# Kernel optimization log

Hardware: AMD Instinct MI355X
Metric: run time of the kernel (lower is better)

## Reference

```python
import jax, jax.numpy as jnp
import numpy as np

HEADS = 16
HEAD_DIM = 64
DIM = 1024
INNER = HEADS * HEAD_DIM  # 1024


def rotate_half(t):
    # split last dim into two halves, return cat(-x2, x1)
    x1, x2 = jnp.split(t, 2, axis=-1)
    return jnp.concatenate((-x2, x1), axis=-1)


def rope_table(n, head_dim, dtype):
    inv_freq = 1.0 / (10000.0 ** (jnp.arange(0, head_dim, 2, dtype=jnp.float32) / head_dim))
    freqs = jnp.arange(n, dtype=jnp.float32)[:, None] * inv_freq[None, :]  # [n, hd/2]
    return jnp.concatenate((freqs, freqs), axis=-1).astype(dtype)  # [n, hd]


def setup_inputs() -> dict:
    key = jax.random.key(0)
    k1, k2, k3, k4 = jax.random.split(key, 4)
    x = jax.random.normal(k1, (1, 4096, DIM), dtype=jnp.float32)
    s = 0.02
    W_qkv = jax.random.normal(k2, (DIM, 3 * INNER), dtype=jnp.float32) * s
    W_o1 = jax.random.normal(k3, (INNER, DIM), dtype=jnp.float32) * s
    W_o2 = jax.random.normal(k4, (DIM, DIM), dtype=jnp.float32) * s
    gamma = jnp.ones((DIM,), dtype=jnp.float32)
    return {"x": x, "W_qkv": W_qkv, "W_o1": W_o1, "W_o2": W_o2, "gamma": gamma}


def reference(x, W_qkv, W_o1, W_o2, gamma):
    b, n, _ = x.shape
    scale = HEAD_DIM ** -0.5
    qkv = x @ W_qkv  # [b, n, 3*inner]
    q, k, v = jnp.split(qkv, 3, axis=-1)
    # [b, n, inner] -> [b, h, n, hd]
    to_heads = lambda t: t.reshape(b, n, HEADS, HEAD_DIM).transpose(0, 2, 1, 3)
    q, k, v = to_heads(q), to_heads(k), to_heads(v)

    pos = rope_table(n, HEAD_DIM, x.dtype)  # [n, hd]
    cos, sin = jnp.cos(pos), jnp.sin(pos)
    apply_rope = lambda t: t * cos + rotate_half(t) * sin
    q, k = apply_rope(q), apply_rope(k)

    dots = jnp.einsum('bhid,bhjd->bhij', q, k) * scale  # [b, h, n, n]
    causal = jnp.triu(jnp.ones((n, n), dtype=bool), 1)
    neg = -jnp.finfo(dots.dtype).max
    dots = jnp.where(causal, neg, dots)
    attn = jax.nn.softmax(dots, axis=-1)

    out = jnp.einsum('bhij,bhjd->bhid', attn, v)  # [b, h, n, hd]
    out = out.transpose(0, 2, 1, 3).reshape(b, n, INNER)
    # to_out: Linear -> ReLU -> Linear (dropout = identity in eval)
    out = jax.nn.relu(out @ W_o1) @ W_o2
    # AttnLayerNorm: layer_norm over last dim with gamma, beta=0
    mean = jnp.mean(out, axis=-1, keepdims=True)
    var = jnp.var(out, axis=-1, keepdims=True)
    out = (out - mean) * jax.lax.rsqrt(var + 1e-5) * gamma
    return out
```

## Files before the change

### kernel.cpp

```cpp
#include <hip/hip_runtime.h>
#include <hip/hip_bf16.h>
#include <float.h>
#include <math.h>

#define HEADS 16
#define HD 64
#define DIM 1024
#define NTOK 4096
#define QKVN 3072

typedef short s8v __attribute__((ext_vector_type(8)));
typedef float f4v __attribute__((ext_vector_type(4)));

static __device__ __forceinline__ unsigned short f2b(float f) {
  __hip_bfloat16 h = __float2bfloat16(f);
  unsigned short u;
  __builtin_memcpy(&u, &h, 2);
  return u;
}
static __device__ __forceinline__ s8v pack_bf8(float4 a, float4 b) {
  s8v r;
  r[0] = (short)f2b(a.x); r[1] = (short)f2b(a.y); r[2] = (short)f2b(a.z); r[3] = (short)f2b(a.w);
  r[4] = (short)f2b(b.x); r[5] = (short)f2b(b.y); r[6] = (short)f2b(b.z); r[7] = (short)f2b(b.w);
  return r;
}

__global__ __launch_bounds__(256) void transpose_f2b(const float* __restrict__ in,
                                                     unsigned short* __restrict__ out,
                                                     int K, int N) {
  __shared__ unsigned short T[32][36];
  const int k0 = blockIdx.y * 32, n0 = blockIdx.x * 32;
  const int t = threadIdx.x;
  const int r = t >> 3, c4 = (t & 7) * 4;
  float4 f = *(const float4*)(in + (size_t)(k0 + r) * N + n0 + c4);
  T[r][c4 + 0] = f2b(f.x);
  T[r][c4 + 1] = f2b(f.y);
  T[r][c4 + 2] = f2b(f.z);
  T[r][c4 + 3] = f2b(f.w);
  __syncthreads();
  ushort4 o;
  o.x = T[c4 + 0][r];
  o.y = T[c4 + 1][r];
  o.z = T[c4 + 2][r];
  o.w = T[c4 + 3][r];
  *(ushort4*)(out + (size_t)(n0 + r) * K + k0 + c4) = o;
}

template <int OUT_F32, int RELU>
__global__ __launch_bounds__(256) void gemm_bt(const float* __restrict__ A,
                                               const unsigned short* __restrict__ Bt,
                                               void* __restrict__ Cv,
                                               int M, int N, int K) {
  __shared__ unsigned short As[128][40];
  __shared__ unsigned short Bs[128][40];
  const int t = threadIdx.x;
  const int wave = t >> 6, lane = t & 63;
  const int wr = wave >> 1, wc = wave & 1;
  const int g = lane >> 4, c = lane & 15;
  const int m0 = blockIdx.y * 128, n0 = blockIdx.x * 128;

  const int sr = t >> 2;
  const int sc = (t & 3) * 8;

  f4v acc[4][4] = {};

  for (int k0 = 0; k0 < K; k0 += 32) {
    const float* p0 = A + (size_t)(m0 + sr) * K + k0 + sc;
    const float* p1 = A + (size_t)(m0 + sr + 64) * K + k0 + sc;
    s8v a0 = pack_bf8(*(const float4*)p0, *(const float4*)(p0 + 4));
    s8v a1 = pack_bf8(*(const float4*)p1, *(const float4*)(p1 + 4));
    s8v b0 = *(const s8v*)(Bt + (size_t)(n0 + sr) * K + k0 + sc);
    s8v b1 = *(const s8v*)(Bt + (size_t)(n0 + sr + 64) * K + k0 + sc);
    __syncthreads();
    *(s8v*)&As[sr][sc] = a0;
    *(s8v*)&As[sr + 64][sc] = a1;
    *(s8v*)&Bs[sr][sc] = b0;
    *(s8v*)&Bs[sr + 64][sc] = b1;
    __syncthreads();
    s8v af[4], bf[4];
#pragma unroll
    for (int m = 0; m < 4; ++m) af[m] = *(const s8v*)&As[wr * 64 + m * 16 + c][g * 8];
#pragma unroll
    for (int n = 0; n < 4; ++n) bf[n] = *(const s8v*)&Bs[wc * 64 + n * 16 + c][g * 8];
#pragma unroll
    for (int m = 0; m < 4; ++m)
#pragma unroll
      for (int n = 0; n < 4; ++n)
        acc[m][n] = __builtin_amdgcn_mfma_f32_16x16x32_bf16(af[m], bf[n], acc[m][n], 0, 0, 0);
  }

#pragma unroll
  for (int m = 0; m < 4; ++m)
#pragma unroll
    for (int n = 0; n < 4; ++n)
#pragma unroll
      for (int r = 0; r < 4; ++r) {
        const int row = m0 + wr * 64 + m * 16 + g * 4 + r;
        const int col = n0 + wc * 64 + n * 16 + c;
        float v = acc[m][n][r];
        if (RELU) v = fmaxf(v, 0.f);
        if (OUT_F32)
          ((float*)Cv)[(size_t)row * N + col] = v;
        else
          ((unsigned short*)Cv)[(size_t)row * N + col] = f2b(v);
      }
}

__global__ __launch_bounds__(512) void rope64_kernel(unsigned short* __restrict__ qkv) {
  __shared__ float cs[32], sn[32];
  const int i = blockIdx.x;
  const int t = threadIdx.x;
  if (t < 32) {
    const double inv = pow(10000.0, -(double)t / 32.0);
    double sd, cd;
    sincos((double)i * inv, &sd, &cd);
    cs[t] = (float)cd;
    sn[t] = (float)sd;
  }
  __syncthreads();
  const int h = t >> 5, j = t & 31;
  const float cc = cs[j], ss = sn[j];
  const size_t base = (size_t)i * QKVN + h * HD + j;
  const float qa = __bfloat162float(*(const __hip_bfloat16*)&qkv[base]);
  const float qb = __bfloat162float(*(const __hip_bfloat16*)&qkv[base + 32]);
  qkv[base] = f2b(qa * cc - qb * ss);
  qkv[base + 32] = f2b(qb * cc + qa * ss);
  const float ka = __bfloat162float(*(const __hip_bfloat16*)&qkv[base + DIM]);
  const float kb = __bfloat162float(*(const __hip_bfloat16*)&qkv[base + DIM + 32]);
  qkv[base + DIM] = f2b(ka * cc - kb * ss);
  qkv[base + DIM + 32] = f2b(kb * cc + ka * ss);
}

__global__ __launch_bounds__(256) void attn_mfma(const unsigned short* __restrict__ qkv,
                                                 float* __restrict__ att) {
  __shared__ unsigned short Ks[64][72];
  __shared__ unsigned short Vt[64][72];
  __shared__ unsigned short Pl[4][16][72];
  const int bid = blockIdx.x;
  const int h = bid & 15;
  const int qi = 63 - (bid >> 4);
  const int t = threadIdx.x;
  const int w = t >> 6, lane = t & 63;
  const int g = lane >> 4, c = lane & 15;
  const int q0 = qi * 64 + w * 16;

  s8v qf[2];
#pragma unroll
  for (int kf = 0; kf < 2; ++kf)
    qf[kf] = *(const s8v*)(qkv + (size_t)(q0 + c) * QKVN + h * HD + kf * 32 + g * 8);

  f4v O[4] = {};
  float mrow[4], lrow[4];
#pragma unroll
  for (int r = 0; r < 4; ++r) { mrow[r] = -1e30f; lrow[r] = 0.f; }

  const int ntile = qi + 1;
  for (int tile = 0; tile < ntile; ++tile) {
    const int kv0 = tile * 64;
    __syncthreads();
    {
      const int kr = t >> 3;
      const int kc = (t & 7) * 8;
#pragma unroll
      for (int it = 0; it < 2; ++it) {
        const int r = kr + it * 32;
        *(s8v*)&Ks[r][kc] =
            *(const s8v*)(qkv + (size_t)(kv0 + r) * QKVN + DIM + h * HD + kc);
      }
      const int kg = t & 15, dc = t >> 4;
      const unsigned short* vb = qkv + (size_t)(kv0 + 4 * kg) * QKVN + 2 * DIM + h * HD + dc * 4;
      ushort4 v0 = *(const ushort4*)(vb);
      ushort4 v1 = *(const ushort4*)(vb + QKVN);
      ushort4 v2 = *(const ushort4*)(vb + 2 * QKVN);
      ushort4 v3 = *(const ushort4*)(vb + 3 * QKVN);
      const unsigned short* r0 = (const unsigned short*)&v0;
      const unsigned short* r1 = (const unsigned short*)&v1;
      const unsigned short* r2 = (const unsigned short*)&v2;
      const unsigned short* r3 = (const unsigned short*)&v3;
#pragma unroll
      for (int dl = 0; dl < 4; ++dl) {
        ushort4 u;
        u.x = r0[dl]; u.y = r1[dl]; u.z = r2[dl]; u.w = r3[dl];
        *(ushort4*)&Vt[dc * 4 + dl][kg * 4] = u;
      }
    }
    __syncthreads();

    f4v S[4] = {};
#pragma unroll
    for (int n = 0; n < 4; ++n)
#pragma unroll
      for (int kf = 0; kf < 2; ++kf) {
        s8v kfr = *(const s8v*)&Ks[n * 16 + c][kf * 32 + g * 8];
        S[n] = __builtin_amdgcn_mfma_f32_16x16x32_bf16(qf[kf], kfr, S[n], 0, 0, 0);
      }

    float rmax[4] = {-1e30f, -1e30f, -1e30f, -1e30f};
#pragma unroll
    for (int n = 0; n < 4; ++n)
#pragma unroll
      for (int r = 0; r < 4; ++r) {
        float s = S[n][r] * 0.125f;
        const int col = kv0 + n * 16 + c;
        const int row = q0 + 4 * g + r;
        s = (col > row) ? -1e30f : s;
        S[n][r] = s;
        rmax[r] = fmaxf(rmax[r], s);
      }
#pragma unroll
    for (int r = 0; r < 4; ++r) {
      rmax[r] = fmaxf(rmax[r], __shfl_xor(rmax[r], 1));
      rmax[r] = fmaxf(rmax[r], __shfl_xor(rmax[r], 2));
      rmax[r] = fmaxf(rmax[r], __shfl_xor(rmax[r], 4));
      rmax[r] = fmaxf(rmax[r], __shfl_xor(rmax[r], 8));
    }

    float corr[4], rsum[4] = {0.f, 0.f, 0.f, 0.f};
#pragma unroll
    for (int r = 0; r < 4; ++r) {
      const float mn = fmaxf(mrow[r], rmax[r]);
      corr[r] = __expf(mrow[r] - mn);
      mrow[r] = mn;
    }
#pragma unroll
    for (int n = 0; n < 4; ++n)
#pragma unroll
      for (int r = 0; r < 4; ++r) {
        const float p = __expf(S[n][r] - mrow[r]);
        rsum[r] += p;
        Pl[w][4 * g + r][n * 16 + c] = f2b(p);
      }
#pragma unroll
    for (int r = 0; r < 4; ++r) {
      rsum[r] += __shfl_xor(rsum[r], 1);
      rsum[r] += __shfl_xor(rsum[r], 2);
      rsum[r] += __shfl_xor(rsum[r], 4);
      rsum[r] += __shfl_xor(rsum[r], 8);
      lrow[r] = lrow[r] * corr[r] + rsum[r];
    }
#pragma unroll
    for (int n = 0; n < 4; ++n)
#pragma unroll
      for (int r = 0; r < 4; ++r) O[n][r] *= corr[r];

    s8v pf[2];
#pragma unroll
    for (int kf = 0; kf < 2; ++kf) pf[kf] = *(const s8v*)&Pl[w][c][kf * 32 + g * 8];
#pragma unroll
    for (int n = 0; n < 4; ++n)
#pragma unroll
      for (int kf = 0; kf < 2; ++kf) {
        s8v vf = *(const s8v*)&Vt[n * 16 + c][kf * 32 + g * 8];
        O[n] = __builtin_amdgcn_mfma_f32_16x16x32_bf16(pf[kf], vf, O[n], 0, 0, 0);
      }
  }

  float inv[4];
#pragma unroll
  for (int r = 0; r < 4; ++r) inv[r] = 1.f / lrow[r];
#pragma unroll
  for (int n = 0; n < 4; ++n)
#pragma unroll
    for (int r = 0; r < 4; ++r) {
      const int row = q0 + 4 * g + r;
      att[(size_t)row * DIM + h * HD + n * 16 + c] = O[n][r] * inv[r];
    }
}

__global__ __launch_bounds__(256) void layernorm_kernel(const float* __restrict__ x,
                                                        const float* __restrict__ gamma,
                                                        float* __restrict__ out) {
  const int row = blockIdx.x;
  const int t = threadIdx.x;
  const float4 v = ((const float4*)(x + (size_t)row * DIM))[t];
  float s = v.x + v.y + v.z + v.w;
  float ss = v.x * v.x + v.y * v.y + v.z * v.z + v.w * v.w;
#pragma unroll
  for (int off = 32; off > 0; off >>= 1) {
    s += __shfl_xor(s, off);
    ss += __shfl_xor(ss, off);
  }
  __shared__ float red[8];
  const int wave = t >> 6, lane = t & 63;
  if (lane == 0) {
    red[wave] = s;
    red[4 + wave] = ss;
  }
  __syncthreads();
  const float S = red[0] + red[1] + red[2] + red[3];
  const float SS = red[4] + red[5] + red[6] + red[7];
  const float mean = S * (1.f / 1024.f);
  const float var = SS * (1.f / 1024.f) - mean * mean;
  const float r = rsqrtf(var + 1e-5f);
  const float4 g4 = ((const float4*)gamma)[t];
  float4 o;
  o.x = (v.x - mean) * r * g4.x;
  o.y = (v.y - mean) * r * g4.y;
  o.z = (v.z - mean) * r * g4.z;
  o.w = (v.w - mean) * r * g4.w;
  ((float4*)(out + (size_t)row * DIM))[t] = o;
}

extern "C" void kernel_launch(void* const* d_in, const int* in_sizes, int n_in,
                              void* d_out, int out_size, void* d_ws, size_t ws_size,
                              hipStream_t stream) {
  const float* x = (const float*)d_in[0];
  const float* Wqkv = (const float*)d_in[1];
  const float* Wo1 = (const float*)d_in[2];
  const float* Wo2 = (const float*)d_in[3];
  const float* gamma = (const float*)d_in[4];
  float* out = (float*)d_out;

  char* wsb = (char*)d_ws;
  unsigned short* qkv = (unsigned short*)wsb;
  unsigned short* Wqkvt = (unsigned short*)(wsb + 25165824ull);
  unsigned short* Wo1t = (unsigned short*)(wsb + 31457280ull);
  unsigned short* Wo2t = (unsigned short*)(wsb + 33554432ull);
  float* h1 = (float*)wsb;
  float* h2 = (float*)(wsb + 16777216ull);
  float* att = out;

  transpose_f2b<<<dim3(QKVN / 32, DIM / 32), 256, 0, stream>>>(Wqkv, Wqkvt, DIM, QKVN);
  transpose_f2b<<<dim3(DIM / 32, DIM / 32), 256, 0, stream>>>(Wo1, Wo1t, DIM, DIM);
  transpose_f2b<<<dim3(DIM / 32, DIM / 32), 256, 0, stream>>>(Wo2, Wo2t, DIM, DIM);
  gemm_bt<0, 0><<<dim3(QKVN / 128, NTOK / 128), 256, 0, stream>>>(x, Wqkvt, qkv, NTOK, QKVN, DIM);
  rope64_kernel<<<NTOK, 512, 0, stream>>>(qkv);
  attn_mfma<<<NTOK / 64 * HEADS, 256, 0, stream>>>(qkv, att);
  gemm_bt<1, 1><<<dim3(DIM / 128, NTOK / 128), 256, 0, stream>>>(att, Wo1t, h1, NTOK, DIM, DIM);
  gemm_bt<1, 0><<<dim3(DIM / 128, NTOK / 128), 256, 0, stream>>>(h1, Wo2t, h2, NTOK, DIM, DIM);
  layernorm_kernel<<<NTOK, 256, 0, stream>>>(h2, gamma, out);
}
```

Baseline: 359.4 us.

## Use bf16 activations, direct-to-LDS GEMM loads, and lazy softmax rescaling

Casts x to bf16 up front and keeps the attention output and the first MLP activation in bf16. This lets every GEMM use bf16 A operands loaded with global_load_lds straight into unpadded shared memory. The attention scale is folded into Q during RoPE, causal masking is skipped for off-diagonal tiles, and the online-softmax rescale only runs when the row max grows by more than a threshold. Together these cut memory traffic, conversion work and VALU work. In exchange it adds bf16 rounding of the intermediates and risks LDS bank conflicts from dropping the padding.

```diff
diff --git a/kernel.cpp b/kernel.cpp
--- a/kernel.cpp
+++ b/kernel.cpp
@@ -23,6 +23,19 @@
   r[0] = (short)f2b(a.x); r[1] = (short)f2b(a.y); r[2] = (short)f2b(a.z); r[3] = (short)f2b(a.w);
   r[4] = (short)f2b(b.x); r[5] = (short)f2b(b.y); r[6] = (short)f2b(b.z); r[7] = (short)f2b(b.w);
   return r;
+}
+static __device__ __forceinline__ void gload16(const unsigned short* g, unsigned short* l) {
+  __builtin_amdgcn_global_load_lds(
+      (const __attribute__((address_space(1))) void*)g,
+      (__attribute__((address_space(3))) void*)l, 16, 0, 0);
+}
+
+__global__ __launch_bounds__(256) void cast_f2b(const float* __restrict__ in,
+                                                unsigned short* __restrict__ out) {
+  const int i = (blockIdx.x * 256 + threadIdx.x) * 8;
+  float4 a = *(const float4*)(in + i);
+  float4 b = *(const float4*)(in + i + 4);
+  *(s8v*)(out + i) = pack_bf8(a, b);
 }
 
 __global__ __launch_bounds__(256) void transpose_f2b(const float* __restrict__ in,
@@ -47,12 +60,12 @@
 }
 
 template <int OUT_F32, int RELU>
-__global__ __launch_bounds__(256) void gemm_bt(const float* __restrict__ A,
+__global__ __launch_bounds__(256) void gemm_bb(const unsigned short* __restrict__ A,
                                                const unsigned short* __restrict__ Bt,
                                                void* __restrict__ Cv,
                                                int M, int N, int K) {
-  __shared__ unsigned short As[128][40];
-  __shared__ unsigned short Bs[128][40];
+  __shared__ __align__(16) unsigned short As[128 * 32];
+  __shared__ __align__(16) unsigned short Bs[128 * 32];
   const int t = threadIdx.x;
   const int wave = t >> 6, lane = t & 63;
   const int wr = wave >> 1, wc = wave & 1;
@@ -62,26 +75,29 @@
   const int sr = t >> 2;
   const int sc = (t & 3) * 8;
 
+  const unsigned short* a0p = A + (size_t)(m0 + sr) * K + sc;
+  const unsigned short* a1p = A + (size_t)(m0 + sr + 64) * K + sc;
+  const unsigned short* b0p = Bt + (size_t)(n0 + sr) * K + sc;
+  const unsigned short* b1p = Bt + (size_t)(n0 + sr + 64) * K + sc;
+  unsigned short* lA0 = As + t * 8;
+  unsigned short* lA1 = As + 2048 + t * 8;
+  unsigned short* lB0 = Bs + t * 8;
+  unsigned short* lB1 = Bs + 2048 + t * 8;
+
   f4v acc[4][4] = {};
 
   for (int k0 = 0; k0 < K; k0 += 32) {
-    const float* p0 = A + (size_t)(m0 + sr) * K + k0 + sc;
-    const float* p1 = A + (size_t)(m0 + sr + 64) * K + k0 + sc;
-    s8v a0 = pack_bf8(*(const float4*)p0, *(const float4*)(p0 + 4));
-    s8v a1 = pack_bf8(*(const float4*)p1, *(const float4*)(p1 + 4));
-    s8v b0 = *(const s8v*)(Bt + (size_t)(n0 + sr) * K + k0 + sc);
-    s8v b1 = *(const s8v*)(Bt + (size_t)(n0 + sr + 64) * K + k0 + sc);
     __syncthreads();
-    *(s8v*)&As[sr][sc] = a0;
-    *(s8v*)&As[sr + 64][sc] = a1;
-    *(s8v*)&Bs[sr][sc] = b0;
-    *(s8v*)&Bs[sr + 64][sc] = b1;
+    gload16(a0p + k0, lA0);
+    gload16(a1p + k0, lA1);
+    gload16(b0p + k0, lB0);
+    gload16(b1p + k0, lB1);
     __syncthreads();
     s8v af[4], bf[4];
 #pragma unroll
-    for (int m = 0; m < 4; ++m) af[m] = *(const s8v*)&As[wr * 64 + m * 16 + c][g * 8];
-#pragma unroll
-    for (int n = 0; n < 4; ++n) bf[n] = *(const s8v*)&Bs[wc * 64 + n * 16 + c][g * 8];
+    for (int m = 0; m < 4; ++m) af[m] = *(const s8v*)&As[(wr * 64 + m * 16 + c) * 32 + g * 8];
+#pragma unroll
+    for (int n = 0; n < 4; ++n) bf[n] = *(const s8v*)&Bs[(wc * 64 + n * 16 + c) * 32 + g * 8];
 #pragma unroll
     for (int m = 0; m < 4; ++m)
 #pragma unroll
@@ -123,8 +139,8 @@
   const size_t base = (size_t)i * QKVN + h * HD + j;
   const float qa = __bfloat162float(*(const __hip_bfloat16*)&qkv[base]);
   const float qb = __bfloat162float(*(const __hip_bfloat16*)&qkv[base + 32]);
-  qkv[base] = f2b(qa * cc - qb * ss);
-  qkv[base + 32] = f2b(qb * cc + qa * ss);
+  qkv[base] = f2b((qa * cc - qb * ss) * 0.125f);
+  qkv[base + 32] = f2b((qb * cc + qa * ss) * 0.125f);
   const float ka = __bfloat162float(*(const __hip_bfloat16*)&qkv[base + DIM]);
   const float kb = __bfloat162float(*(const __hip_bfloat16*)&qkv[base + DIM + 32]);
   qkv[base + DIM] = f2b(ka * cc - kb * ss);
@@ -132,7 +148,7 @@
 }
 
 __global__ __launch_bounds__(256) void attn_mfma(const unsigned short* __restrict__ qkv,
-                                                 float* __restrict__ att) {
+                                                 unsigned short* __restrict__ att) {
   __shared__ unsigned short Ks[64][72];
   __shared__ unsigned short Vt[64][72];
   __shared__ unsigned short Pl[4][16][72];
@@ -196,17 +212,24 @@
       }
 
     float rmax[4] = {-1e30f, -1e30f, -1e30f, -1e30f};
-#pragma unroll
-    for (int n = 0; n < 4; ++n)
-#pragma unroll
-      for (int r = 0; r < 4; ++r) {
-        float s = S[n][r] * 0.125f;
-        const int col = kv0 + n * 16 + c;
-        const int row = q0 + 4 * g + r;
-        s = (col > row) ? -1e30f : s;
-        S[n][r] = s;
-        rmax[r] = fmaxf(rmax[r], s);
-      }
+    if (kv0 + 63 > q0) {
+#pragma unroll
+      for (int n = 0; n < 4; ++n)
+#pragma unroll
+        for (int r = 0; r < 4; ++r) {
+          float s = S[n][r];
+          const int col = kv0 + n * 16 + c;
+          const int row = q0 + 4 * g + r;
+          s = (col > row) ? -1e30f : s;
+          S[n][r] = s;
+          rmax[r] = fmaxf(rmax[r], s);
+        }
+    } else {
+#pragma unroll
+      for (int n = 0; n < 4; ++n)
+#pragma unroll
+        for (int r = 0; r < 4; ++r) rmax[r] = fmaxf(rmax[r], S[n][r]);
+    }
 #pragma unroll
     for (int r = 0; r < 4; ++r) {
       rmax[r] = fmaxf(rmax[r], __shfl_xor(rmax[r], 1));
@@ -215,13 +238,21 @@
       rmax[r] = fmaxf(rmax[r], __shfl_xor(rmax[r], 8));
     }
 
-    float corr[4], rsum[4] = {0.f, 0.f, 0.f, 0.f};
-#pragma unroll
-    for (int r = 0; r < 4; ++r) {
-      const float mn = fmaxf(mrow[r], rmax[r]);
-      corr[r] = __expf(mrow[r] - mn);
-      mrow[r] = mn;
-    }
+    bool upd = false;
+#pragma unroll
+    for (int r = 0; r < 4; ++r) upd = upd || (rmax[r] > mrow[r] + 8.0f);
+    if (__any((int)upd)) {
+#pragma unroll
+      for (int r = 0; r < 4; ++r) {
+        const float mn = fmaxf(mrow[r], rmax[r]);
+        const float corr = __expf(mrow[r] - mn);
+        mrow[r] = mn;
+        lrow[r] *= corr;
+#pragma unroll
+        for (int n = 0; n < 4; ++n) O[n][r] *= corr;
+      }
+    }
+    float rsum[4] = {0.f, 0.f, 0.f, 0.f};
 #pragma unroll
     for (int n = 0; n < 4; ++n)
 #pragma unroll
@@ -236,12 +267,8 @@
       rsum[r] += __shfl_xor(rsum[r], 2);
       rsum[r] += __shfl_xor(rsum[r], 4);
       rsum[r] += __shfl_xor(rsum[r], 8);
-      lrow[r] = lrow[r] * corr[r] + rsum[r];
-    }
-#pragma unroll
-    for (int n = 0; n < 4; ++n)
-#pragma unroll
-      for (int r = 0; r < 4; ++r) O[n][r] *= corr[r];
+      lrow[r] += rsum[r];
+    }
 
     s8v pf[2];
 #pragma unroll
@@ -263,7 +290,7 @@
 #pragma unroll
     for (int r = 0; r < 4; ++r) {
       const int row = q0 + 4 * g + r;
-      att[(size_t)row * DIM + h * HD + n * 16 + c] = O[n][r] * inv[r];
+      att[(size_t)row * DIM + h * HD + n * 16 + c] = f2b(O[n][r] * inv[r]);
     }
 }
 
@@ -312,21 +339,23 @@
   float* out = (float*)d_out;
 
   char* wsb = (char*)d_ws;
-  unsigned short* qkv = (unsigned short*)wsb;
-  unsigned short* Wqkvt = (unsigned short*)(wsb + 25165824ull);
-  unsigned short* Wo1t = (unsigned short*)(wsb + 31457280ull);
-  unsigned short* Wo2t = (unsigned short*)(wsb + 33554432ull);
-  float* h1 = (float*)wsb;
+  unsigned short* xb = (unsigned short*)wsb;
+  unsigned short* qkv = (unsigned short*)(wsb + 8388608ull);
+  unsigned short* Wqkvt = (unsigned short*)(wsb + 33554432ull);
+  unsigned short* Wo1t = (unsigned short*)(wsb + 39845888ull);
+  unsigned short* Wo2t = (unsigned short*)(wsb + 41943040ull);
+  unsigned short* att = (unsigned short*)wsb;
+  unsigned short* h1 = (unsigned short*)(wsb + 8388608ull);
   float* h2 = (float*)(wsb + 16777216ull);
-  float* att = out;
-
+
+  cast_f2b<<<NTOK * DIM / (256 * 8), 256, 0, stream>>>(x, xb);
   transpose_f2b<<<dim3(QKVN / 32, DIM / 32), 256, 0, stream>>>(Wqkv, Wqkvt, DIM, QKVN);
   transpose_f2b<<<dim3(DIM / 32, DIM / 32), 256, 0, stream>>>(Wo1, Wo1t, DIM, DIM);
   transpose_f2b<<<dim3(DIM / 32, DIM / 32), 256, 0, stream>>>(Wo2, Wo2t, DIM, DIM);
-  gemm_bt<0, 0><<<dim3(QKVN / 128, NTOK / 128), 256, 0, stream>>>(x, Wqkvt, qkv, NTOK, QKVN, DIM);
+  gemm_bb<0, 0><<<dim3(QKVN / 128, NTOK / 128), 256, 0, stream>>>(xb, Wqkvt, qkv, NTOK, QKVN, DIM);
   rope64_kernel<<<NTOK, 512, 0, stream>>>(qkv);
   attn_mfma<<<NTOK / 64 * HEADS, 256, 0, stream>>>(qkv, att);
-  gemm_bt<1, 1><<<dim3(DIM / 128, NTOK / 128), 256, 0, stream>>>(att, Wo1t, h1, NTOK, DIM, DIM);
-  gemm_bt<1, 0><<<dim3(DIM / 128, NTOK / 128), 256, 0, stream>>>(h1, Wo2t, h2, NTOK, DIM, DIM);
+  gemm_bb<0, 1><<<dim3(DIM / 128, NTOK / 128), 256, 0, stream>>>(att, Wo1t, h1, NTOK, DIM, DIM);
+  gemm_bb<1, 0><<<dim3(DIM / 128, NTOK / 128), 256, 0, stream>>>(h1, Wo2t, h2, NTOK, DIM, DIM);
   layernorm_kernel<<<NTOK, 256, 0, stream>>>(h2, gamma, out);
 }
```

After: 343.6 us. 1.05x faster.
